# Kernel optimization log

Measured on AMD Instinct MI355X. Metric: run time of the kernel, lower is better.

The kernel has to match this reference:

```python
import jax, jax.numpy as jnp
import numpy as np

DIM = 512
NUM_HEADS = 1
WS = 16
B, H, W = 2, WS * WS, 1


def _rel_pos_index(ws):
    # matches Attention.calculate_relative_position_index (no Swin offset -> negatives)
    coords = np.stack(np.meshgrid(np.arange(ws), np.arange(ws), indexing='ij'), 0).reshape(2, -1)
    rel = coords[:, :, None] - coords[:, None, :]          # [2, ws^2, ws^2]
    return rel.transpose(1, 2, 0).sum(-1)                  # [ws^2, ws^2] in [-(2ws-2), 2ws-2]

_NTAB = (2 * WS - 1) ** 2
# torch fancy indexing wraps negative indices; emulate with mod (values are in (-NTAB, NTAB))
_RPI = np.mod(_rel_pos_index(WS), _NTAB).reshape(-1)       # [ws^4]


def setup_inputs() -> dict:
    key = jax.random.key(0)
    ks = jax.random.split(key, 6)
    x = jax.random.normal(ks[0], (B, DIM, H, W), dtype=jnp.float32)
    qkv_w = jax.random.normal(ks[1], (3 * DIM, DIM), dtype=jnp.float32) * (DIM ** -0.5)
    qkv_b = jax.random.normal(ks[2], (3 * DIM,), dtype=jnp.float32) * 0.02
    proj_w = jax.random.normal(ks[3], (DIM, DIM), dtype=jnp.float32) * (DIM ** -0.5)
    proj_b = jax.random.normal(ks[4], (DIM,), dtype=jnp.float32) * 0.02
    rpb = jax.random.normal(ks[5], (_NTAB, NUM_HEADS), dtype=jnp.float32) * 0.02
    return {"x": x, "qkv_w": qkv_w, "qkv_b": qkv_b,
            "proj_w": proj_w, "proj_b": proj_b, "rpb": rpb}


def reference(x, qkv_w, qkv_b, proj_w, proj_b, rpb):
    b, c, h, w = x.shape                                   # [B, C, H, W=1]
    d = c // NUM_HEADS
    scale = d ** -0.5                                      # qk_scale=None -> (dim//nh)^-0.5
    # 1x1 conv == channel matmul
    qkv = jnp.einsum('bchw,oc->bohw', x, qkv_w) + qkv_b[None, :, None, None]
    qkv = qkv.reshape(b, 3, NUM_HEADS, d, h, w)
    q, k, v = qkv[:, 0], qkv[:, 1], qkv[:, 2]              # [B, nh, d, H, W]
    # matmul over last two dims: contracts W -> [B, nh, d, H, H]
    attn = jnp.einsum('bndhw,bndgw->bndhg', q, k) * scale
    idx = jnp.asarray(_RPI)
    bias = rpb[idx].reshape(h * w, h * w, -1).transpose(2, 0, 1)  # [nh, HW, HW] = [1, H, H]
    attn = jax.nn.softmax(attn + bias, axis=-1)
    out = jnp.einsum('bndhg,bndgw->bndhw', attn, v).sum(axis=1)   # sum over heads -> [B, d, H, W]
    out = jnp.einsum('bchw,oc->bohw', out, proj_w) + proj_b[None, :, None, None]
    return out
```

## Files before the change

### kernel.cpp

```cpp
#include <hip/hip_runtime.h>
#include <hip/hip_bf16.h>


#define TOK   256
#define KDIM  512
#define LOG2E 1.4426950408889634f
#define SCALE 0.04419417382415922f
#define NPART 8
#define QPSTRIDE 786432
#define PPSTRIDE 262144

#define EXP2(x) __builtin_amdgcn_exp2f(x)

template<int BM, int KSPLIT>
__global__ __launch_bounds__(256)
void gemm_f32(const float* __restrict__ A, const float* __restrict__ B,
              float* __restrict__ C, int M)
{
    constexpr int KLEN  = KDIM / KSPLIT;
    constexpr int NITER = KLEN / 16;
    constexpr int MM    = BM / 16;
    constexpr int LDA   = BM + 4;

    __shared__ float As[2][16][LDA];
    __shared__ float Bs[2][16][64];

    const int t  = threadIdx.x;
    const int o0 = blockIdx.x * BM;
    const int n0 = blockIdx.y * 64;
    const int b  = blockIdx.z & 1;
    const int ks = blockIdx.z >> 1;

    const float* Ab = A + (size_t)o0 * KDIM + ks * KLEN;
    const float* Bb = B + ((size_t)b * KDIM + (size_t)ks * KLEN) * TOK + n0;
    float*       Cb = C + ((size_t)blockIdx.z * M + o0) * TOK + n0;

    const int ar  = t >> 2;
    const int ac4 = (t & 3) * 4;
    const int bk  = t >> 4;
    const int bn4 = (t & 15) * 4;

    float4 ra0, ra1, rb;
#define LOAD_TILE(IT) do {                                                   \
        const int k0_ = (IT) * 16;                                           \
        ra0 = *(const float4*)(Ab + (size_t)ar * KDIM + k0_ + ac4);          \
        if (BM == 128)                                                       \
            ra1 = *(const float4*)(Ab + (size_t)(64 + ar) * KDIM + k0_ + ac4);\
        rb  = *(const float4*)(Bb + (size_t)(k0_ + bk) * TOK + bn4);         \
    } while (0)
#define STORE_TILE(BUF) do {                                                 \
        As[BUF][ac4 + 0][ar] = ra0.x;                                        \
        As[BUF][ac4 + 1][ar] = ra0.y;                                        \
        As[BUF][ac4 + 2][ar] = ra0.z;                                        \
        As[BUF][ac4 + 3][ar] = ra0.w;                                        \
        if (BM == 128) {                                                     \
            As[BUF][ac4 + 0][64 + ar] = ra1.x;                               \
            As[BUF][ac4 + 1][64 + ar] = ra1.y;                               \
            As[BUF][ac4 + 2][64 + ar] = ra1.z;                               \
            As[BUF][ac4 + 3][64 + ar] = ra1.w;                               \
        }                                                                    \
        *(float4*)&Bs[BUF][bk][bn4] = rb;                                    \
    } while (0)

    const int m0 = (t >> 4) * MM;
    const int n4 = (t & 15) * 4;

    float acc[MM][4];
#pragma unroll
    for (int i = 0; i < MM; ++i)
#pragma unroll
        for (int j = 0; j < 4; ++j) acc[i][j] = 0.f;

    LOAD_TILE(0);
    STORE_TILE(0);
    if (NITER > 1) LOAD_TILE(1);
    __syncthreads();

#pragma unroll
    for (int it = 0; it < NITER; ++it) {
        const int cur = it & 1;
        if (it + 1 < NITER) STORE_TILE(1 - cur);
        if (it + 2 < NITER) LOAD_TILE(it + 2);
#pragma unroll
        for (int kk = 0; kk < 16; ++kk) {
            const float4 b4 = *(const float4*)&Bs[cur][kk][n4];
            float af[MM];
#pragma unroll
            for (int mi = 0; mi < MM; mi += 4) {
                const float4 a4 = *(const float4*)&As[cur][kk][m0 + mi];
                af[mi + 0] = a4.x; af[mi + 1] = a4.y;
                af[mi + 2] = a4.z; af[mi + 3] = a4.w;
            }
#pragma unroll
            for (int mi = 0; mi < MM; ++mi) {
                acc[mi][0] = fmaf(af[mi], b4.x, acc[mi][0]);
                acc[mi][1] = fmaf(af[mi], b4.y, acc[mi][1]);
                acc[mi][2] = fmaf(af[mi], b4.z, acc[mi][2]);
                acc[mi][3] = fmaf(af[mi], b4.w, acc[mi][3]);
            }
        }
        __syncthreads();
    }

#pragma unroll
    for (int mi = 0; mi < MM; ++mi) {
        const float4 o4 = make_float4(acc[mi][0], acc[mi][1], acc[mi][2], acc[mi][3]);
        *(float4*)(Cb + (size_t)(m0 + mi) * TOK + n4) = o4;
    }
#undef LOAD_TILE
#undef STORE_TILE
}

__global__ __launch_bounds__(256)
void attn_f32(const float* __restrict__ qkvp, const float* __restrict__ qkv_b,
              const float* __restrict__ rpb, float* __restrict__ aout)
{
    __shared__ float ks_[2][TOK];
    __shared__ float vs_[2][TOK];
    __shared__ float tab2[64];
    __shared__ float brow[31][258];
    __shared__ float lpart[2][TOK];
    __shared__ float apart[2][TOK];

    const int t  = threadIdx.x;
    const int b  = blockIdx.y;
    const int d0 = blockIdx.x * 2;
    const float* q0 = qkvp + (size_t)b * (1536 * TOK);

    if (t < 61) {
        const int rel = t - 30;
        tab2[t] = rpb[rel < 0 ? rel + 961 : rel] * LOG2E;
    }
    {
        const int sel = t >> 7;
        const int row = (t >> 6) & 1;
        const int g4  = (t & 63) * 4;
        const int o   = (sel ? 1024 : 512) + d0 + row;
        const float* p = q0 + (size_t)o * TOK + g4;
        const float bb = qkv_b[o];
        float4 v = make_float4(bb, bb, bb, bb);
#pragma unroll
        for (int pp = 0; pp < NPART; ++pp) {
            const float4 x = *(const float4*)(p + (size_t)pp * QPSTRIDE);
            v.x += x.x; v.y += x.y; v.z += x.z; v.w += x.w;
        }
        if (sel == 0) {
            const float s = SCALE * LOG2E;
            v.x *= s; v.y *= s; v.z *= s; v.w *= s;
            *(float4*)&ks_[row][g4] = v;
        } else {
            *(float4*)&vs_[row][g4] = v;
        }
    }
    __syncthreads();
    {
        const int rg = ((t >> 4) & 15) + (t & 15);
#pragma unroll 1
        for (int it = 0; it < 31; ++it)
            brow[it][t] = tab2[it - rg + 30];
    }
    __syncthreads();

    const int w   = t >> 6;
    const int dl  = w & 1;
    const int gh  = w >> 1;
    const int hl  = t & 63;
    const int qi  = ((hl & 15) << 2) | (hl >> 4);
    const int h0  = qi * 4;
    const int rh0 = (qi >> 2) + 4 * (qi & 3);

    float q[4];
    {
        const float* p = q0 + (size_t)(d0 + dl) * TOK + h0;
        const float bb = qkv_b[d0 + dl];
        q[0] = bb; q[1] = bb; q[2] = bb; q[3] = bb;
#pragma unroll
        for (int pp = 0; pp < NPART; ++pp) {
            const float4 x = *(const float4*)(p + (size_t)pp * QPSTRIDE);
            q[0] += x.x; q[1] += x.y; q[2] += x.z; q[3] += x.w;
        }
    }

    float l[4]  = {0.f, 0.f, 0.f, 0.f};
    float am[4] = {0.f, 0.f, 0.f, 0.f};

    const int pbeg = gh * 128;
#pragma unroll 2
    for (int p = pbeg; p < pbeg + 128; p += 4) {
        const float4 k4 = *(const float4*)&ks_[dl][p];
        const float4 v4 = *(const float4*)&vs_[dl][p];
#pragma unroll
        for (int r = 0; r < 4; ++r) {
            const float2 b01 = *(const float2*)&brow[rh0 + r][p];
            const float2 b23 = *(const float2*)&brow[rh0 + r][p + 2];
            float e;
            e = EXP2(fmaf(q[r], k4.x, b01.x)); l[r] += e; am[r] = fmaf(e, v4.x, am[r]);
            e = EXP2(fmaf(q[r], k4.y, b01.y)); l[r] += e; am[r] = fmaf(e, v4.y, am[r]);
            e = EXP2(fmaf(q[r], k4.z, b23.x)); l[r] += e; am[r] = fmaf(e, v4.z, am[r]);
            e = EXP2(fmaf(q[r], k4.w, b23.y)); l[r] += e; am[r] = fmaf(e, v4.w, am[r]);
        }
    }

    if (gh == 1) {
        *(float4*)&lpart[dl][h0] = make_float4(l[0], l[1], l[2], l[3]);
        *(float4*)&apart[dl][h0] = make_float4(am[0], am[1], am[2], am[3]);
    }
    __syncthreads();
    if (gh == 0) {
        const float4 lo = *(const float4*)&lpart[dl][h0];
        const float4 ao = *(const float4*)&apart[dl][h0];
        float4 o4;
        o4.x = (am[0] + ao.x) / (l[0] + lo.x);
        o4.y = (am[1] + ao.y) / (l[1] + lo.y);
        o4.z = (am[2] + ao.z) / (l[2] + lo.z);
        o4.w = (am[3] + ao.w) / (l[3] + lo.w);
        *(float4*)(aout + ((size_t)b * 512 + d0 + dl) * TOK + h0) = o4;
    }
}

__global__ __launch_bounds__(256)
void combine_f32(const float* __restrict__ pp, const float* __restrict__ pb,
                 float* __restrict__ out)
{
    const int gid  = blockIdx.x * 256 + threadIdx.x;
    const int flat = gid * 4;
    const int o = (flat >> 8) & 511;
    float4 a = make_float4(pb[o], pb[o], pb[o], pb[o]);
#pragma unroll
    for (int p = 0; p < NPART; ++p) {
        const float4 x = *(const float4*)(pp + (size_t)p * PPSTRIDE + flat);
        a.x += x.x; a.y += x.y; a.z += x.z; a.w += x.w;
    }
    *(float4*)(out + flat) = a;
}

extern "C" void kernel_launch(void* const* d_in, const int* in_sizes, int n_in,
                              void* d_out, int out_size, void* d_ws, size_t ws_size,
                              hipStream_t stream)
{
    const float* x      = (const float*)d_in[0];
    const float* qkv_w  = (const float*)d_in[1];
    const float* qkv_b  = (const float*)d_in[2];
    const float* proj_w = (const float*)d_in[3];
    const float* proj_b = (const float*)d_in[4];
    const float* rpb    = (const float*)d_in[5];
    float* out = (float*)d_out;
    float* ws  = (float*)d_ws;

    float* qkvp  = ws;
    float* aout  = ws + 6291456;
    float* projp = ws + 6553600;

    gemm_f32<128, 8><<<dim3(12, 4, 16), 256, 0, stream>>>(qkv_w, x, qkvp, 1536);

    attn_f32<<<dim3(256, 2), 256, 0, stream>>>(qkvp, qkv_b, rpb, aout);

    gemm_f32<64, 8><<<dim3(8, 4, 16), 256, 0, stream>>>(proj_w, aout, projp, 512);

    combine_f32<<<dim3(256), 256, 0, stream>>>(projp, proj_b, out);
}
```

Baseline: 105.7 us.

## Replace FP32 SIMT GEMMs with split-bf16 MFMA GEMMs and reduce K-split

Both 1x1-conv GEMMs now run on MFMA bf16 instructions. Each fp32 operand is split into a high and a low bf16 part, and three products are accumulated to keep close to fp32 accuracy. The K-split factor drops from 8 to 2 for the QKV GEMM and from 8 to 4 for the projection GEMM, which shrinks partial-sum traffic and the reduction work in the attention and combine kernels. In exchange, there is conversion work in the shared-memory store, less overlap between loads and compute (a single LDS buffer with two syncs per tile), and fewer blocks for parallelism.

```diff
diff --git a/kernel.cpp b/kernel.cpp
--- a/kernel.cpp
+++ b/kernel.cpp
@@ -1,112 +1,201 @@
 #include <hip/hip_runtime.h>
-#include <hip/hip_bf16.h>
-
-
-#define TOK   256
-#define KDIM  512
-#define LOG2E 1.4426950408889634f
-#define SCALE 0.04419417382415922f
-#define NPART 8
+
+
+#define TOK    256
+#define KDIM   512
+#define LOG2E  1.4426950408889634f
+#define SCALE  0.04419417382415922f
+#define QPARTS 2
+#define PPARTS 4
 #define QPSTRIDE 786432
 #define PPSTRIDE 262144
 
 #define EXP2(x) __builtin_amdgcn_exp2f(x)
 
+typedef __attribute__((ext_vector_type(8))) short short8_t;
+typedef __attribute__((ext_vector_type(4))) float f32x4;
+
+__device__ __forceinline__ unsigned short f2bf(float x) {
+    unsigned int u = __float_as_uint(x);
+    u += 0x7fffu + ((u >> 16) & 1u);
+    return (unsigned short)(u >> 16);
+}
+__device__ __forceinline__ float bf2f(unsigned short h) {
+    return __uint_as_float((unsigned int)h << 16);
+}
+
 template<int BM, int KSPLIT>
 __global__ __launch_bounds__(256)
-void gemm_f32(const float* __restrict__ A, const float* __restrict__ B,
-              float* __restrict__ C, int M)
+void gemm_mfma(const float* __restrict__ A, const float* __restrict__ Bmat,
+               float* __restrict__ C, int M)
 {
-    constexpr int KLEN  = KDIM / KSPLIT;
-    constexpr int NITER = KLEN / 16;
-    constexpr int MM    = BM / 16;
-    constexpr int LDA   = BM + 4;
-
-    __shared__ float As[2][16][LDA];
-    __shared__ float Bs[2][16][64];
+    constexpr int KLEN = KDIM / KSPLIT;
+    constexpr int NT   = KLEN / 64;
+    constexpr int MF   = BM / 32;
+    constexpr int AP   = BM / 16;
+    constexpr int SA   = 72;
+    constexpr int SB   = 68;
+
+    __shared__ unsigned short As_h[BM * SA];
+    __shared__ unsigned short As_l[BM * SA];
+    __shared__ unsigned int   Bs[64 * SB];
 
     const int t  = threadIdx.x;
     const int o0 = blockIdx.x * BM;
     const int n0 = blockIdx.y * 64;
-    const int b  = blockIdx.z & 1;
-    const int ks = blockIdx.z >> 1;
+    const int z  = blockIdx.z;
+    const int b  = z & 1;
+    const int ks = z >> 1;
 
     const float* Ab = A + (size_t)o0 * KDIM + ks * KLEN;
-    const float* Bb = B + ((size_t)b * KDIM + (size_t)ks * KLEN) * TOK + n0;
-    float*       Cb = C + ((size_t)blockIdx.z * M + o0) * TOK + n0;
-
-    const int ar  = t >> 2;
-    const int ac4 = (t & 3) * 4;
-    const int bk  = t >> 4;
-    const int bn4 = (t & 15) * 4;
-
-    float4 ra0, ra1, rb;
-#define LOAD_TILE(IT) do {                                                   \
-        const int k0_ = (IT) * 16;                                           \
-        ra0 = *(const float4*)(Ab + (size_t)ar * KDIM + k0_ + ac4);          \
-        if (BM == 128)                                                       \
-            ra1 = *(const float4*)(Ab + (size_t)(64 + ar) * KDIM + k0_ + ac4);\
-        rb  = *(const float4*)(Bb + (size_t)(k0_ + bk) * TOK + bn4);         \
+    const float* Bb = Bmat + ((size_t)b * KDIM + (size_t)ks * KLEN) * TOK + n0;
+    float*       Cb = C + ((size_t)z * M + o0) * TOK + n0;
+
+    const int ak4 = (t & 15) * 4;
+    const int am  = t >> 4;
+    const int btt = t & 63;
+    const int bc4 = (t >> 6) * 4;
+
+    float4 pa[AP];
+    float  pb[16];
+
+#define LOAD_TILE(KT) do {                                                    \
+        const float* ap_ = Ab + (KT) * 64 + ak4;                              \
+        _Pragma("unroll")                                                     \
+        for (int p = 0; p < AP; ++p)                                          \
+            pa[p] = *(const float4*)(ap_ + (size_t)(am + 16 * p) * KDIM);     \
+        const float* bp_ = Bb + (size_t)(KT) * 64 * TOK + btt;                \
+        _Pragma("unroll")                                                     \
+        for (int p = 0; p < 4; ++p)                                           \
+            _Pragma("unroll")                                                 \
+            for (int j = 0; j < 4; ++j)                                       \
+                pb[p * 4 + j] = bp_[(size_t)(bc4 + p * 16 + j) * TOK];        \
     } while (0)
-#define STORE_TILE(BUF) do {                                                 \
-        As[BUF][ac4 + 0][ar] = ra0.x;                                        \
-        As[BUF][ac4 + 1][ar] = ra0.y;                                        \
-        As[BUF][ac4 + 2][ar] = ra0.z;                                        \
-        As[BUF][ac4 + 3][ar] = ra0.w;                                        \
-        if (BM == 128) {                                                     \
-            As[BUF][ac4 + 0][64 + ar] = ra1.x;                               \
-            As[BUF][ac4 + 1][64 + ar] = ra1.y;                               \
-            As[BUF][ac4 + 2][64 + ar] = ra1.z;                               \
-            As[BUF][ac4 + 3][64 + ar] = ra1.w;                               \
-        }                                                                    \
-        *(float4*)&Bs[BUF][bk][bn4] = rb;                                    \
+
+#define STORE_TILE() do {                                                     \
+        _Pragma("unroll")                                                     \
+        for (int p = 0; p < AP; ++p) {                                        \
+            const int m_ = am + 16 * p;                                       \
+            const float4 v_ = pa[p];                                          \
+            const unsigned short h0 = f2bf(v_.x), h1 = f2bf(v_.y),            \
+                                 h2 = f2bf(v_.z), h3 = f2bf(v_.w);            \
+            const unsigned short l0 = f2bf(v_.x - bf2f(h0)),                  \
+                                 l1 = f2bf(v_.y - bf2f(h1)),                  \
+                                 l2 = f2bf(v_.z - bf2f(h2)),                  \
+                                 l3 = f2bf(v_.w - bf2f(h3));                  \
+            *(ushort4*)&As_h[(size_t)m_ * SA + ak4] =                         \
+                make_ushort4(h0, h1, h2, h3);                                 \
+            *(ushort4*)&As_l[(size_t)m_ * SA + ak4] =                         \
+                make_ushort4(l0, l1, l2, l3);                                 \
+        }                                                                     \
+        _Pragma("unroll")                                                     \
+        for (int p = 0; p < 4; ++p) {                                         \
+            unsigned int wv0, wv1, wv2, wv3;                                  \
+            {                                                                 \
+                const float x0 = pb[p * 4 + 0], x1 = pb[p * 4 + 1],           \
+                            x2 = pb[p * 4 + 2], x3 = pb[p * 4 + 3];           \
+                const unsigned short a0 = f2bf(x0), a1 = f2bf(x1),            \
+                                     a2 = f2bf(x2), a3 = f2bf(x3);            \
+                wv0 = (unsigned int)a0 |                                      \
+                      ((unsigned int)f2bf(x0 - bf2f(a0)) << 16);              \
+                wv1 = (unsigned int)a1 |                                      \
+                      ((unsigned int)f2bf(x1 - bf2f(a1)) << 16);              \
+                wv2 = (unsigned int)a2 |                                      \
+                      ((unsigned int)f2bf(x2 - bf2f(a2)) << 16);              \
+                wv3 = (unsigned int)a3 |                                      \
+                      ((unsigned int)f2bf(x3 - bf2f(a3)) << 16);              \
+            }                                                                 \
+            *(uint4*)&Bs[(size_t)btt * SB + bc4 + p * 16] =                   \
+                make_uint4(wv0, wv1, wv2, wv3);                               \
+        }                                                                     \
     } while (0)
 
-    const int m0 = (t >> 4) * MM;
-    const int n4 = (t & 15) * 4;
-
-    float acc[MM][4];
-#pragma unroll
-    for (int i = 0; i < MM; ++i)
-#pragma unroll
-        for (int j = 0; j < 4; ++j) acc[i][j] = 0.f;
+    const int wid  = t >> 6;
+    const int wm   = wid & 1;
+    const int wn   = wid >> 1;
+    const int lane = t & 63;
+    const int lr   = lane & 15;
+    const int lg   = lane >> 4;
+
+    const int mwb = wm * (BM / 2);
+    const int nwb = wn * 32;
+
+    f32x4 acc[MF][2];
+#pragma unroll
+    for (int mi = 0; mi < MF; ++mi)
+#pragma unroll
+        for (int ni = 0; ni < 2; ++ni)
+            acc[mi][ni] = (f32x4){0.f, 0.f, 0.f, 0.f};
 
     LOAD_TILE(0);
-    STORE_TILE(0);
-    if (NITER > 1) LOAD_TILE(1);
+    STORE_TILE();
     __syncthreads();
 
 #pragma unroll
-    for (int it = 0; it < NITER; ++it) {
-        const int cur = it & 1;
-        if (it + 1 < NITER) STORE_TILE(1 - cur);
-        if (it + 2 < NITER) LOAD_TILE(it + 2);
-#pragma unroll
-        for (int kk = 0; kk < 16; ++kk) {
-            const float4 b4 = *(const float4*)&Bs[cur][kk][n4];
-            float af[MM];
-#pragma unroll
-            for (int mi = 0; mi < MM; mi += 4) {
-                const float4 a4 = *(const float4*)&As[cur][kk][m0 + mi];
-                af[mi + 0] = a4.x; af[mi + 1] = a4.y;
-                af[mi + 2] = a4.z; af[mi + 3] = a4.w;
+    for (int kt = 0; kt < NT; ++kt) {
+        if (kt + 1 < NT) LOAD_TILE(kt + 1);
+
+#pragma unroll
+        for (int ksp = 0; ksp < 2; ++ksp) {
+            const int kb = ksp * 32 + lg * 8;
+
+            short8_t ah[MF], al[MF];
+#pragma unroll
+            for (int mi = 0; mi < MF; ++mi) {
+                const int m_ = mwb + mi * 16 + lr;
+                ah[mi] = *(const short8_t*)&As_h[(size_t)m_ * SA + kb];
+                al[mi] = *(const short8_t*)&As_l[(size_t)m_ * SA + kb];
             }
-#pragma unroll
-            for (int mi = 0; mi < MM; ++mi) {
-                acc[mi][0] = fmaf(af[mi], b4.x, acc[mi][0]);
-                acc[mi][1] = fmaf(af[mi], b4.y, acc[mi][1]);
-                acc[mi][2] = fmaf(af[mi], b4.z, acc[mi][2]);
-                acc[mi][3] = fmaf(af[mi], b4.w, acc[mi][3]);
+
+            short8_t bh[2], bl[2];
+#pragma unroll
+            for (int ni = 0; ni < 2; ++ni) {
+                const unsigned int* wp =
+                    &Bs[(size_t)(nwb + ni * 16 + lr) * SB + kb];
+                const uint4 w0 = *(const uint4*)wp;
+                const uint4 w1 = *(const uint4*)(wp + 4);
+                short8_t h_, l_;
+                h_[0] = (short)(w0.x & 0xffffu); l_[0] = (short)(w0.x >> 16);
+                h_[1] = (short)(w0.y & 0xffffu); l_[1] = (short)(w0.y >> 16);
+                h_[2] = (short)(w0.z & 0xffffu); l_[2] = (short)(w0.z >> 16);
+                h_[3] = (short)(w0.w & 0xffffu); l_[3] = (short)(w0.w >> 16);
+                h_[4] = (short)(w1.x & 0xffffu); l_[4] = (short)(w1.x >> 16);
+                h_[5] = (short)(w1.y & 0xffffu); l_[5] = (short)(w1.y >> 16);
+                h_[6] = (short)(w1.z & 0xffffu); l_[6] = (short)(w1.z >> 16);
+                h_[7] = (short)(w1.w & 0xffffu); l_[7] = (short)(w1.w >> 16);
+                bh[ni] = h_; bl[ni] = l_;
             }
-        }
-        __syncthreads();
-    }
-
-#pragma unroll
-    for (int mi = 0; mi < MM; ++mi) {
-        const float4 o4 = make_float4(acc[mi][0], acc[mi][1], acc[mi][2], acc[mi][3]);
-        *(float4*)(Cb + (size_t)(m0 + mi) * TOK + n4) = o4;
-    }
+
+#pragma unroll
+            for (int mi = 0; mi < MF; ++mi)
+#pragma unroll
+                for (int ni = 0; ni < 2; ++ni) {
+                    acc[mi][ni] = __builtin_amdgcn_mfma_f32_16x16x32_bf16(
+                        ah[mi], bh[ni], acc[mi][ni], 0, 0, 0);
+                    acc[mi][ni] = __builtin_amdgcn_mfma_f32_16x16x32_bf16(
+                        al[mi], bh[ni], acc[mi][ni], 0, 0, 0);
+                    acc[mi][ni] = __builtin_amdgcn_mfma_f32_16x16x32_bf16(
+                        ah[mi], bl[ni], acc[mi][ni], 0, 0, 0);
+                }
+        }
+
+        if (kt + 1 < NT) {
+            __syncthreads();
+            STORE_TILE();
+            __syncthreads();
+        }
+    }
+
+#pragma unroll
+    for (int mi = 0; mi < MF; ++mi)
+#pragma unroll
+        for (int ni = 0; ni < 2; ++ni)
+#pragma unroll
+            for (int r = 0; r < 4; ++r) {
+                const int row = mwb + mi * 16 + lg * 4 + r;
+                const int col = nwb + ni * 16 + lr;
+                Cb[(size_t)row * TOK + col] = acc[mi][ni][r];
+            }
 #undef LOAD_TILE
 #undef STORE_TILE
 }
@@ -140,7 +229,7 @@
         const float bb = qkv_b[o];
         float4 v = make_float4(bb, bb, bb, bb);
 #pragma unroll
-        for (int pp = 0; pp < NPART; ++pp) {
+        for (int pp = 0; pp < QPARTS; ++pp) {
             const float4 x = *(const float4*)(p + (size_t)pp * QPSTRIDE);
             v.x += x.x; v.y += x.y; v.z += x.z; v.w += x.w;
         }
@@ -175,7 +264,7 @@
         const float bb = qkv_b[d0 + dl];
         q[0] = bb; q[1] = bb; q[2] = bb; q[3] = bb;
 #pragma unroll
-        for (int pp = 0; pp < NPART; ++pp) {
+        for (int pp = 0; pp < QPARTS; ++pp) {
             const float4 x = *(const float4*)(p + (size_t)pp * QPSTRIDE);
             q[0] += x.x; q[1] += x.y; q[2] += x.z; q[3] += x.w;
         }
@@ -227,7 +316,7 @@
     const int o = (flat >> 8) & 511;
     float4 a = make_float4(pb[o], pb[o], pb[o], pb[o]);
 #pragma unroll
-    for (int p = 0; p < NPART; ++p) {
+    for (int p = 0; p < PPARTS; ++p) {
         const float4 x = *(const float4*)(pp + (size_t)p * PPSTRIDE + flat);
         a.x += x.x; a.y += x.y; a.z += x.z; a.w += x.w;
     }
@@ -248,14 +337,14 @@
     float* ws  = (float*)d_ws;
 
     float* qkvp  = ws;
-    float* aout  = ws + 6291456;
-    float* projp = ws + 6553600;
-
-    gemm_f32<128, 8><<<dim3(12, 4, 16), 256, 0, stream>>>(qkv_w, x, qkvp, 1536);
+    float* aout  = ws + 1572864;
+    float* projp = ws + 1835008;
+
+    gemm_mfma<128, 2><<<dim3(12, 4, 4), 256, 0, stream>>>(qkv_w, x, qkvp, 1536);
 
     attn_f32<<<dim3(256, 2), 256, 0, stream>>>(qkvp, qkv_b, rpb, aout);
 
-    gemm_f32<64, 8><<<dim3(8, 4, 16), 256, 0, stream>>>(proj_w, aout, projp, 512);
+    gemm_mfma<64, 4><<<dim3(8, 4, 8), 256, 0, stream>>>(proj_w, aout, projp, 512);
 
     combine_f32<<<dim3(256), 256, 0, stream>>>(projp, proj_b, out);
 }
```

After: 97.35 us (median of 2 runs). 7.9% less time.

## Replace fp32 SIMT GEMMs with split-bf16 MFMA GEMMs on pre-packed fragments

Applied to the files above, without the earlier changes.

Adds a prep kernel that splits the weights and input into high/low bf16 pairs and packs them into an MFMA fragment layout. Both GEMMs then use three bf16 MFMA products per tile (hi*hi, lo*hi, hi*lo) to approximate fp32 accuracy, with no split-K. This removes the combine kernel and the partial-sum reductions. The attention kernel now writes its output directly as packed bf16 hi/lo fragments for the projection GEMM. Weights are re-converted on every call, which adds a prep launch and extra memory traffic, and the split-bf16 scheme gives up a little precision compared with fp32.

```diff
diff --git a/kernel.cpp b/kernel.cpp
--- a/kernel.cpp
+++ b/kernel.cpp
@@ -1,119 +1,167 @@
 #include <hip/hip_runtime.h>
-#include <hip/hip_bf16.h>
-
-
-#define TOK   256
-#define KDIM  512
-#define LOG2E 1.4426950408889634f
-#define SCALE 0.04419417382415922f
-#define NPART 8
-#define QPSTRIDE 786432
-#define PPSTRIDE 262144
+
+
+#define TOK    256
+#define KDIM   512
+#define K8     64
+#define LOG2E  1.4426950408889634f
+#define SCALE  0.04419417382415922f
+
+#define OFF_WQAH 0
+#define OFF_WQAL 786432
+#define OFF_XBH  1572864
+#define OFF_XBL  1835008
+#define OFF_WPAH 2097152
+#define OFF_WPAL 2359296
+#define OFF_AOBH 2621440
+#define OFF_AOBL 2883584
+#define OFF_QKVF 1572864
 
 #define EXP2(x) __builtin_amdgcn_exp2f(x)
 
-template<int BM, int KSPLIT>
+typedef __attribute__((ext_vector_type(8))) short short8_t;
+typedef __attribute__((ext_vector_type(4))) float f32x4;
+
+__device__ __forceinline__ unsigned short f2bf(float x) {
+    unsigned int u = __float_as_uint(x);
+    u += 0x7fffu + ((u >> 16) & 1u);
+    return (unsigned short)(u >> 16);
+}
+__device__ __forceinline__ float bf2f(unsigned short h) {
+    return __uint_as_float((unsigned int)h << 16);
+}
+
+__device__ __forceinline__ void cvt8(const float* v, unsigned short* hq,
+                                     unsigned short* lq) {
+#pragma unroll
+    for (int j = 0; j < 8; ++j) {
+        const unsigned short h = f2bf(v[j]);
+        hq[j] = h;
+        lq[j] = f2bf(v[j] - bf2f(h));
+    }
+}
+
 __global__ __launch_bounds__(256)
-void gemm_f32(const float* __restrict__ A, const float* __restrict__ B,
-              float* __restrict__ C, int M)
-{
-    constexpr int KLEN  = KDIM / KSPLIT;
-    constexpr int NITER = KLEN / 16;
-    constexpr int MM    = BM / 16;
-    constexpr int LDA   = BM + 4;
-
-    __shared__ float As[2][16][LDA];
-    __shared__ float Bs[2][16][64];
-
-    const int t  = threadIdx.x;
-    const int o0 = blockIdx.x * BM;
-    const int n0 = blockIdx.y * 64;
-    const int b  = blockIdx.z & 1;
-    const int ks = blockIdx.z >> 1;
-
-    const float* Ab = A + (size_t)o0 * KDIM + ks * KLEN;
-    const float* Bb = B + ((size_t)b * KDIM + (size_t)ks * KLEN) * TOK + n0;
-    float*       Cb = C + ((size_t)blockIdx.z * M + o0) * TOK + n0;
-
-    const int ar  = t >> 2;
-    const int ac4 = (t & 3) * 4;
-    const int bk  = t >> 4;
-    const int bn4 = (t & 15) * 4;
-
-    float4 ra0, ra1, rb;
-#define LOAD_TILE(IT) do {                                                   \
-        const int k0_ = (IT) * 16;                                           \
-        ra0 = *(const float4*)(Ab + (size_t)ar * KDIM + k0_ + ac4);          \
-        if (BM == 128)                                                       \
-            ra1 = *(const float4*)(Ab + (size_t)(64 + ar) * KDIM + k0_ + ac4);\
-        rb  = *(const float4*)(Bb + (size_t)(k0_ + bk) * TOK + bn4);         \
+void prep(const float* __restrict__ qkv_w, const float* __restrict__ x,
+          const float* __restrict__ proj_w, unsigned short* __restrict__ U)
+{
+    const int id = blockIdx.x * 256 + threadIdx.x;
+    alignas(16) unsigned short hq[8], lq[8];
+    float v[8];
+
+    if (id < 98304) {
+        const int m = id >> 6, kc = id & 63;
+        const float* s = qkv_w + (size_t)m * KDIM + kc * 8;
+#pragma unroll
+        for (int j = 0; j < 8; ++j) v[j] = s[j];
+        cvt8(v, hq, lq);
+        const size_t o = ((size_t)(m >> 4) * K8 + kc) * 128 + (size_t)(m & 15) * 8;
+        *(uint4*)(U + OFF_WQAH + o) = *(const uint4*)hq;
+        *(uint4*)(U + OFF_WQAL + o) = *(const uint4*)lq;
+    } else if (id < 131072) {
+        const int rid = id - 98304;
+        const int n = rid & 255, kc = (rid >> 8) & 63, b = rid >> 14;
+        const float* s = x + ((size_t)b * KDIM + kc * 8) * TOK + n;
+#pragma unroll
+        for (int j = 0; j < 8; ++j) v[j] = s[(size_t)j * TOK];
+        cvt8(v, hq, lq);
+        const size_t o = (((size_t)b * 16 + (n >> 4)) * K8 + kc) * 128
+                         + (size_t)(n & 15) * 8;
+        *(uint4*)(U + OFF_XBH + o) = *(const uint4*)hq;
+        *(uint4*)(U + OFF_XBL + o) = *(const uint4*)lq;
+    } else if (id < 163840) {
+        const int rid = id - 131072;
+        const int m = rid >> 6, kc = rid & 63;
+        const float* s = proj_w + (size_t)m * KDIM + kc * 8;
+#pragma unroll
+        for (int j = 0; j < 8; ++j) v[j] = s[j];
+        cvt8(v, hq, lq);
+        const size_t o = ((size_t)(m >> 4) * K8 + kc) * 128 + (size_t)(m & 15) * 8;
+        *(uint4*)(U + OFF_WPAH + o) = *(const uint4*)hq;
+        *(uint4*)(U + OFF_WPAL + o) = *(const uint4*)lq;
+    }
+}
+
+template<bool BIAS>
+__global__ __launch_bounds__(64)
+void gemm_frag(const unsigned short* __restrict__ Ah,
+               const unsigned short* __restrict__ Al,
+               const unsigned short* __restrict__ Bh,
+               const unsigned short* __restrict__ Bl,
+               const float* __restrict__ bias,
+               float* __restrict__ Cout, int Mtot)
+{
+    const int t   = threadIdx.x;
+    const int lr  = t & 15;
+    const int lg  = t >> 4;
+    const int mt0 = blockIdx.x * 2;
+    const int nt0 = blockIdx.y * 4;
+    const int b   = blockIdx.z;
+
+    f32x4 acc[2][4];
+#pragma unroll
+    for (int mi = 0; mi < 2; ++mi)
+#pragma unroll
+        for (int ni = 0; ni < 4; ++ni)
+            acc[mi][ni] = (f32x4){0.f, 0.f, 0.f, 0.f};
+
+    short8_t ah[2][2], al[2][2], bh[2][4], bl[2][4];
+
+#define LDF(S, P) do {                                                        \
+        const int kc_ = (S) * 4 + lg;                                         \
+        _Pragma("unroll")                                                     \
+        for (int mi = 0; mi < 2; ++mi) {                                      \
+            const size_t o_ = ((size_t)(mt0 + mi) * K8 + kc_) * 128           \
+                              + (size_t)lr * 8;                               \
+            ah[P][mi] = *(const short8_t*)(Ah + o_);                          \
+            al[P][mi] = *(const short8_t*)(Al + o_);                          \
+        }                                                                     \
+        _Pragma("unroll")                                                     \
+        for (int ni = 0; ni < 4; ++ni) {                                      \
+            const size_t o_ = (((size_t)b * 16 + nt0 + ni) * K8 + kc_) * 128  \
+                              + (size_t)lr * 8;                               \
+            bh[P][ni] = *(const short8_t*)(Bh + o_);                          \
+            bl[P][ni] = *(const short8_t*)(Bl + o_);                          \
+        }                                                                     \
     } while (0)
-#define STORE_TILE(BUF) do {                                                 \
-        As[BUF][ac4 + 0][ar] = ra0.x;                                        \
-        As[BUF][ac4 + 1][ar] = ra0.y;                                        \
-        As[BUF][ac4 + 2][ar] = ra0.z;                                        \
-        As[BUF][ac4 + 3][ar] = ra0.w;                                        \
-        if (BM == 128) {                                                     \
-            As[BUF][ac4 + 0][64 + ar] = ra1.x;                               \
-            As[BUF][ac4 + 1][64 + ar] = ra1.y;                               \
-            As[BUF][ac4 + 2][64 + ar] = ra1.z;                               \
-            As[BUF][ac4 + 3][64 + ar] = ra1.w;                               \
-        }                                                                    \
-        *(float4*)&Bs[BUF][bk][bn4] = rb;                                    \
-    } while (0)
-
-    const int m0 = (t >> 4) * MM;
-    const int n4 = (t & 15) * 4;
-
-    float acc[MM][4];
-#pragma unroll
-    for (int i = 0; i < MM; ++i)
-#pragma unroll
-        for (int j = 0; j < 4; ++j) acc[i][j] = 0.f;
-
-    LOAD_TILE(0);
-    STORE_TILE(0);
-    if (NITER > 1) LOAD_TILE(1);
-    __syncthreads();
-
-#pragma unroll
-    for (int it = 0; it < NITER; ++it) {
-        const int cur = it & 1;
-        if (it + 1 < NITER) STORE_TILE(1 - cur);
-        if (it + 2 < NITER) LOAD_TILE(it + 2);
-#pragma unroll
-        for (int kk = 0; kk < 16; ++kk) {
-            const float4 b4 = *(const float4*)&Bs[cur][kk][n4];
-            float af[MM];
-#pragma unroll
-            for (int mi = 0; mi < MM; mi += 4) {
-                const float4 a4 = *(const float4*)&As[cur][kk][m0 + mi];
-                af[mi + 0] = a4.x; af[mi + 1] = a4.y;
-                af[mi + 2] = a4.z; af[mi + 3] = a4.w;
+
+    LDF(0, 0);
+#pragma unroll
+    for (int s = 0; s < 16; ++s) {
+        const int p = s & 1;
+        if (s + 1 < 16) LDF(s + 1, p ^ 1);
+#pragma unroll
+        for (int mi = 0; mi < 2; ++mi)
+#pragma unroll
+            for (int ni = 0; ni < 4; ++ni) {
+                acc[mi][ni] = __builtin_amdgcn_mfma_f32_16x16x32_bf16(
+                    ah[p][mi], bh[p][ni], acc[mi][ni], 0, 0, 0);
+                acc[mi][ni] = __builtin_amdgcn_mfma_f32_16x16x32_bf16(
+                    al[p][mi], bh[p][ni], acc[mi][ni], 0, 0, 0);
+                acc[mi][ni] = __builtin_amdgcn_mfma_f32_16x16x32_bf16(
+                    ah[p][mi], bl[p][ni], acc[mi][ni], 0, 0, 0);
             }
-#pragma unroll
-            for (int mi = 0; mi < MM; ++mi) {
-                acc[mi][0] = fmaf(af[mi], b4.x, acc[mi][0]);
-                acc[mi][1] = fmaf(af[mi], b4.y, acc[mi][1]);
-                acc[mi][2] = fmaf(af[mi], b4.z, acc[mi][2]);
-                acc[mi][3] = fmaf(af[mi], b4.w, acc[mi][3]);
+    }
+#undef LDF
+
+#pragma unroll
+    for (int mi = 0; mi < 2; ++mi)
+#pragma unroll
+        for (int r = 0; r < 4; ++r) {
+            const int row = (mt0 + mi) * 16 + lg * 4 + r;
+            const float pb = BIAS ? bias[row] : 0.f;
+#pragma unroll
+            for (int ni = 0; ni < 4; ++ni) {
+                const int col = (nt0 + ni) * 16 + lr;
+                Cout[((size_t)b * Mtot + row) * TOK + col] = acc[mi][ni][r] + pb;
             }
         }
-        __syncthreads();
-    }
-
-#pragma unroll
-    for (int mi = 0; mi < MM; ++mi) {
-        const float4 o4 = make_float4(acc[mi][0], acc[mi][1], acc[mi][2], acc[mi][3]);
-        *(float4*)(Cb + (size_t)(m0 + mi) * TOK + n4) = o4;
-    }
-#undef LOAD_TILE
-#undef STORE_TILE
 }
 
 __global__ __launch_bounds__(256)
-void attn_f32(const float* __restrict__ qkvp, const float* __restrict__ qkv_b,
-              const float* __restrict__ rpb, float* __restrict__ aout)
+void attn_f32(const float* __restrict__ qkvf, const float* __restrict__ qkv_b,
+              const float* __restrict__ rpb,
+              unsigned short* __restrict__ aoh, unsigned short* __restrict__ aol)
 {
     __shared__ float ks_[2][TOK];
     __shared__ float vs_[2][TOK];
@@ -125,7 +173,7 @@
     const int t  = threadIdx.x;
     const int b  = blockIdx.y;
     const int d0 = blockIdx.x * 2;
-    const float* q0 = qkvp + (size_t)b * (1536 * TOK);
+    const float* q0 = qkvf + (size_t)b * (1536 * TOK);
 
     if (t < 61) {
         const int rel = t - 30;
@@ -136,14 +184,9 @@
         const int row = (t >> 6) & 1;
         const int g4  = (t & 63) * 4;
         const int o   = (sel ? 1024 : 512) + d0 + row;
-        const float* p = q0 + (size_t)o * TOK + g4;
         const float bb = qkv_b[o];
-        float4 v = make_float4(bb, bb, bb, bb);
-#pragma unroll
-        for (int pp = 0; pp < NPART; ++pp) {
-            const float4 x = *(const float4*)(p + (size_t)pp * QPSTRIDE);
-            v.x += x.x; v.y += x.y; v.z += x.z; v.w += x.w;
-        }
+        float4 v = *(const float4*)(q0 + (size_t)o * TOK + g4);
+        v.x += bb; v.y += bb; v.z += bb; v.w += bb;
         if (sel == 0) {
             const float s = SCALE * LOG2E;
             v.x *= s; v.y *= s; v.z *= s; v.w *= s;
@@ -171,14 +214,9 @@
 
     float q[4];
     {
-        const float* p = q0 + (size_t)(d0 + dl) * TOK + h0;
         const float bb = qkv_b[d0 + dl];
-        q[0] = bb; q[1] = bb; q[2] = bb; q[3] = bb;
-#pragma unroll
-        for (int pp = 0; pp < NPART; ++pp) {
-            const float4 x = *(const float4*)(p + (size_t)pp * QPSTRIDE);
-            q[0] += x.x; q[1] += x.y; q[2] += x.z; q[3] += x.w;
-        }
+        const float4 x4 = *(const float4*)(q0 + (size_t)(d0 + dl) * TOK + h0);
+        q[0] = x4.x + bb; q[1] = x4.y + bb; q[2] = x4.z + bb; q[3] = x4.w + bb;
     }
 
     float l[4]  = {0.f, 0.f, 0.f, 0.f};
@@ -209,29 +247,21 @@
     if (gh == 0) {
         const float4 lo = *(const float4*)&lpart[dl][h0];
         const float4 ao = *(const float4*)&apart[dl][h0];
-        float4 o4;
-        o4.x = (am[0] + ao.x) / (l[0] + lo.x);
-        o4.y = (am[1] + ao.y) / (l[1] + lo.y);
-        o4.z = (am[2] + ao.z) / (l[2] + lo.z);
-        o4.w = (am[3] + ao.w) / (l[3] + lo.w);
-        *(float4*)(aout + ((size_t)b * 512 + d0 + dl) * TOK + h0) = o4;
-    }
-}
-
-__global__ __launch_bounds__(256)
-void combine_f32(const float* __restrict__ pp, const float* __restrict__ pb,
-                 float* __restrict__ out)
-{
-    const int gid  = blockIdx.x * 256 + threadIdx.x;
-    const int flat = gid * 4;
-    const int o = (flat >> 8) & 511;
-    float4 a = make_float4(pb[o], pb[o], pb[o], pb[o]);
-#pragma unroll
-    for (int p = 0; p < NPART; ++p) {
-        const float4 x = *(const float4*)(pp + (size_t)p * PPSTRIDE + flat);
-        a.x += x.x; a.y += x.y; a.z += x.z; a.w += x.w;
-    }
-    *(float4*)(out + flat) = a;
+        float vals[4];
+        vals[0] = (am[0] + ao.x) / (l[0] + lo.x);
+        vals[1] = (am[1] + ao.y) / (l[1] + lo.y);
+        vals[2] = (am[2] + ao.z) / (l[2] + lo.z);
+        vals[3] = (am[3] + ao.w) / (l[3] + lo.w);
+        const int d = d0 + dl;
+        const size_t ob = (((size_t)b * 16 + (h0 >> 4)) * K8 + (d >> 3)) * 128
+                          + (size_t)(h0 & 15) * 8 + (d & 7);
+#pragma unroll
+        for (int r = 0; r < 4; ++r) {
+            const unsigned short hh = f2bf(vals[r]);
+            aoh[ob + (size_t)r * 8] = hh;
+            aol[ob + (size_t)r * 8] = f2bf(vals[r] - bf2f(hh));
+        }
+    }
 }
 
 extern "C" void kernel_launch(void* const* d_in, const int* in_sizes, int n_in,
@@ -245,17 +275,20 @@
     const float* proj_b = (const float*)d_in[4];
     const float* rpb    = (const float*)d_in[5];
     float* out = (float*)d_out;
-    float* ws  = (float*)d_ws;
-
-    float* qkvp  = ws;
-    float* aout  = ws + 6291456;
-    float* projp = ws + 6553600;
-
-    gemm_f32<128, 8><<<dim3(12, 4, 16), 256, 0, stream>>>(qkv_w, x, qkvp, 1536);
-
-    attn_f32<<<dim3(256, 2), 256, 0, stream>>>(qkvp, qkv_b, rpb, aout);
-
-    gemm_f32<64, 8><<<dim3(8, 4, 16), 256, 0, stream>>>(proj_w, aout, projp, 512);
-
-    combine_f32<<<dim3(256), 256, 0, stream>>>(projp, proj_b, out);
-}
+
+    unsigned short* U = (unsigned short*)d_ws;
+    float* qkvf = (float*)d_ws + OFF_QKVF;
+
+    prep<<<dim3(640), 256, 0, stream>>>(qkv_w, x, proj_w, U);
+
+    gemm_frag<false><<<dim3(48, 4, 2), 64, 0, stream>>>(
+        U + OFF_WQAH, U + OFF_WQAL, U + OFF_XBH, U + OFF_XBL,
+        nullptr, qkvf, 1536);
+
+    attn_f32<<<dim3(256, 2), 256, 0, stream>>>(qkvf, qkv_b, rpb,
+                                               U + OFF_AOBH, U + OFF_AOBL);
+
+    gemm_frag<true><<<dim3(16, 4, 2), 64, 0, stream>>>(
+        U + OFF_WPAH, U + OFF_WPAL, U + OFF_AOBH, U + OFF_AOBL,
+        proj_b, out, 512);
+}
```

New measurement: 116.0 us. 1.1x slower.
